# Performance work log

Measured on AMD Instinct MI355X. Metric: run time of the kernel, lower is better.

## Reference

```python
import jax, jax.numpy as jnp
import numpy as np

B, H, W, C = 4, 128, 128, 256
D_MODEL, NH = 512, 8
DH = D_MODEL // NH  # 64


def setup_inputs() -> dict:
    key = jax.random.key(0)
    ks = jax.random.split(key, 5)
    s = lambda fan_in: 1.0 / np.sqrt(fan_in)
    return {
        "x": jax.random.normal(ks[0], (B, H, W, C), jnp.float32),
        "Wq": jax.random.normal(ks[1], (C, D_MODEL), jnp.float32) * s(C),
        "bq": jnp.zeros((D_MODEL,), jnp.float32),
        "Wk": jax.random.normal(ks[2], (C, D_MODEL), jnp.float32) * s(C),
        "bk": jnp.zeros((D_MODEL,), jnp.float32),
        "Wv": jax.random.normal(ks[3], (C, D_MODEL), jnp.float32) * s(C),
        "bv": jnp.zeros((D_MODEL,), jnp.float32),
        "Wo": jax.random.normal(ks[4], (D_MODEL, C), jnp.float32) * s(D_MODEL),
        "bo": jnp.zeros((C,), jnp.float32),
    }


def reference(x, Wq, bq, Wk, bk, Wv, bv, Wo, bo):
    # Axial multi-head attention along axis 1 (H), W axis is batched.
    b, h, w, _ = x.shape
    q = (x @ Wq + bq).reshape(b, h, w, NH, DH) * (DH ** -0.5)
    k = (x @ Wk + bk).reshape(b, h, w, NH, DH)
    v = (x @ Wv + bv).reshape(b, h, w, NH, DH)
    # scores over the H axis: [B, Nh, W, H, H]
    scores = jnp.einsum("bxwnd,bywnd->bnwxy", q, k)
    probs = jax.nn.softmax(scores, axis=-1)
    # [B, H, W, Nh, DH] -> [B, H, W, d_model]
    out = jnp.einsum("bnwxy,bywnd->bxwnd", probs, v).reshape(b, h, w, D_MODEL)
    # Wo projection; original combines to [B,W,H,C] then permutes back to [B,H,W,C],
    # which is equivalent to applying Wo directly here. Dropout is identity at inference.
    return out @ Wo + bo
```

## Files before the change

kernel.cpp:

```cpp
#include <hip/hip_runtime.h>

typedef unsigned short u16;
typedef __attribute__((ext_vector_type(8))) short bf16x8;
typedef __attribute__((ext_vector_type(8))) unsigned short u16x8;
typedef __attribute__((ext_vector_type(4))) float f32x4;

#define DEVI static __device__ __forceinline__

DEVI u16 f2b(float f) {
  unsigned u = __builtin_bit_cast(unsigned, f);
  return (u16)((u + 0x7FFFu + ((u >> 16) & 1u)) >> 16);
}

DEVI void gload_lds16(const void* g, void* l) {
  __builtin_amdgcn_global_load_lds(
      (const __attribute__((address_space(1))) unsigned int*)g,
      (__attribute__((address_space(3))) unsigned int*)l, 16, 0, 0);
}


__global__ __launch_bounds__(256) void prep_x(const float* __restrict__ x, u16* __restrict__ xb) {
  const int n8 = 65536 * 256 / 8;
  int i = blockIdx.x * blockDim.x + threadIdx.x;
  for (; i < n8; i += gridDim.x * blockDim.x) {
    const float4* p = (const float4*)x + (size_t)i * 2;
    float4 a = p[0], b = p[1];
    u16x8 r;
    r[0] = f2b(a.x); r[1] = f2b(a.y); r[2] = f2b(a.z); r[3] = f2b(a.w);
    r[4] = f2b(b.x); r[5] = f2b(b.y); r[6] = f2b(b.z); r[7] = f2b(b.w);
    *(u16x8*)(xb + (size_t)i * 8) = r;
  }
}

__global__ __launch_bounds__(256) void prep_w(
    const float* __restrict__ Wq, const float* __restrict__ Wk,
    const float* __restrict__ Wv, const float* __restrict__ Wo,
    const float* __restrict__ bq, const float* __restrict__ bk, const float* __restrict__ bv,
    u16* __restrict__ wqkvT, u16* __restrict__ woT, float* __restrict__ bqkv) {
  const int NW1 = 1536 * 256, NW2 = 256 * 512;
  const int total = NW1 + NW2 + 1536;
  int i = blockIdx.x * blockDim.x + threadIdx.x;
  for (; i < total; i += gridDim.x * blockDim.x) {
    if (i < NW1) {
      int nn = i >> 8, kk = i & 255;
      float v;
      if (nn < 512)       v = Wq[kk * 512 + nn] * 0.125f;
      else if (nn < 1024) v = Wk[kk * 512 + (nn - 512)];
      else                v = Wv[kk * 512 + (nn - 1024)];
      wqkvT[i] = f2b(v);
    } else if (i < NW1 + NW2) {
      int j = i - NW1;
      int nn = j >> 9, kk = j & 511;
      woT[j] = f2b(Wo[kk * 256 + nn]);
    } else {
      int j = i - NW1 - NW2;
      bqkv[j] = (j < 512) ? bq[j] * 0.125f : (j < 1024 ? bk[j - 512] : bv[j - 1024]);
    }
  }
}


template <int KK, bool OUT_BF16>
__global__ __launch_bounds__(1024) void gemm256(
    const u16* __restrict__ A, const u16* __restrict__ Bt,
    const float* __restrict__ bias, void* __restrict__ Cv, int N) {
  constexpr int NT = KK / 64;
  __shared__ u16 smem[65536];
  const int tid = threadIdx.x;
  const int lane = tid & 63, wid = tid >> 6;
  const int nTn = N >> 8;
  const int qx = gridDim.x >> 3;
  const int wg = (blockIdx.x & 7) * qx + (blockIdx.x >> 3);
  const long m0 = (long)(wg / nTn) * 256;
  const long n0 = (long)(wg % nTn) * 256;
  const int wr = wid >> 2, wc = wid & 3;
  const int hi = lane >> 4, lo = lane & 15;
  const u16* Ab = A + m0 * KK;
  const u16* Bb = Bt + n0 * KK;
  const int srow_ = tid >> 3;
  const int schunk = tid & 7;

  f32x4 acc[4][4];
#pragma unroll
  for (int mi = 0; mi < 4; ++mi)
#pragma unroll
    for (int ni = 0; ni < 4; ++ni) acc[mi][ni] = f32x4{0.f, 0.f, 0.f, 0.f};

  auto stage = [&](int t) {
    u16* base = &smem[(t & 1) * 32768];
    const int kt = t * 64;
#pragma unroll
    for (int j = 0; j < 2; ++j) {
      int row = j * 128 + srow_;
      int colE = (schunk ^ (row & 7)) << 3;
      gload_lds16(Ab + (long)row * KK + kt + colE, &base[(j * 1024 + tid) * 8]);
    }
#pragma unroll
    for (int j = 0; j < 2; ++j) {
      int row = j * 128 + srow_;
      int colE = (schunk ^ (row & 7)) << 3;
      gload_lds16(Bb + (long)row * KK + kt + colE, &base[16384 + (j * 1024 + tid) * 8]);
    }
  };

  stage(0);
#pragma unroll
  for (int t = 0; t < NT; ++t) {
    if (t + 1 < NT) {
      stage(t + 1);
      asm volatile("s_waitcnt vmcnt(4)" ::: "memory");
    } else {
      asm volatile("s_waitcnt vmcnt(0)" ::: "memory");
    }
    __builtin_amdgcn_sched_barrier(0);
    __builtin_amdgcn_s_barrier();
    const u16* aB = &smem[(t & 1) * 32768];
    const u16* bB = aB + 16384;
#pragma unroll
    for (int ks = 0; ks < 2; ++ks) {
      const int slot = ((hi + ks * 4) ^ (lo & 7)) << 3;
      bf16x8 af[4], bfr[4];
#pragma unroll
      for (int mi = 0; mi < 4; ++mi)
        af[mi] = *(const bf16x8*)&aB[(wr * 64 + mi * 16 + lo) * 64 + slot];
#pragma unroll
      for (int ni = 0; ni < 4; ++ni)
        bfr[ni] = *(const bf16x8*)&bB[(wc * 64 + ni * 16 + lo) * 64 + slot];
#pragma unroll
      for (int mi = 0; mi < 4; ++mi)
#pragma unroll
        for (int ni = 0; ni < 4; ++ni)
          acc[mi][ni] = __builtin_amdgcn_mfma_f32_16x16x32_bf16(af[mi], bfr[ni], acc[mi][ni], 0, 0, 0);
    }
    __builtin_amdgcn_sched_barrier(0);
    __builtin_amdgcn_s_barrier();
  }

  float bb[4];
#pragma unroll
  for (int ni = 0; ni < 4; ++ni) bb[ni] = bias[n0 + wc * 64 + ni * 16 + lo];

  if (OUT_BF16) {
    u16* Cg = (u16*)Cv;
#pragma unroll
    for (int mi = 0; mi < 4; ++mi)
#pragma unroll
      for (int ni = 0; ni < 4; ++ni) {
#pragma unroll
        for (int j = 0; j < 4; ++j) {
          int row = wr * 64 + mi * 16 + hi * 4 + j;
          int chunk = (wc * 8 + ni * 2 + (lo >> 3)) ^ ((row >> 2) & 7);
          smem[row * 256 + chunk * 8 + (lo & 7)] = f2b(acc[mi][ni][j] + bb[ni]);
        }
      }
    __syncthreads();
#pragma unroll
    for (int it = 0; it < 8; ++it) {
      int idx = it * 1024 + tid;
      int row = idx >> 5, c = idx & 31;
      int cs = c ^ ((row >> 2) & 7);
      *(u16x8*)(Cg + (m0 + row) * N + n0 + c * 8) = *(const u16x8*)&smem[row * 256 + cs * 8];
    }
  } else {
    float* Cg = (float*)Cv;
#pragma unroll
    for (int mi = 0; mi < 4; ++mi)
#pragma unroll
      for (int ni = 0; ni < 4; ++ni) {
        long cg = n0 + wc * 64 + ni * 16 + lo;
#pragma unroll
        for (int j = 0; j < 4; ++j)
          Cg[(m0 + wr * 64 + mi * 16 + hi * 4 + j) * N + cg] = acc[mi][ni][j] + bb[ni];
      }
  }
}


__global__ __launch_bounds__(256) void attn_axial(const u16* __restrict__ qkv,
                                                  u16* __restrict__ ao) {
  __shared__ u16 smem[24576];
  u16* qld = smem;
  u16* kld = smem + 8192;
  u16* vt  = smem + 16384;
  u16* pld = smem;

  const int g = blockIdx.x;
  const int n = g & 7, w = (g >> 3) & 127, b = g >> 10;
  const int tid = threadIdx.x, lane = tid & 63, wid = tid >> 6;
  const size_t ystr = (size_t)128 * 1536;
  const size_t base = (size_t)(b * 16384 + w) * 1536;
  const size_t bq_ = base + n * 64;
  const size_t bk_ = base + 512 + n * 64;
  const size_t bv_ = base + 1024 + n * 64;
  const int srow = lane >> 3, sc = lane & 7;
  const int hi = lane >> 4, lo = lane & 15;

#pragma unroll
  for (int j = 0; j < 4; ++j) {
    int y = wid * 32 + j * 8 + srow;
    gload_lds16(qkv + bq_ + (size_t)y * ystr + sc * 8, &qld[(wid * 32 + j * 8) * 64]);
    gload_lds16(qkv + bk_ + (size_t)y * ystr + sc * 8, &kld[(wid * 32 + j * 8) * 64]);
  }
  {
    const int h2 = tid >> 6;
    const int yp = (tid & 63) * 2;
    const u16* g0 = qkv + bv_ + (size_t)yp * ystr + h2 * 16;
    u16x8 a0 = *(const u16x8*)g0;
    u16x8 a1 = *(const u16x8*)(g0 + 8);
    u16x8 c0 = *(const u16x8*)(g0 + ystr);
    u16x8 c1 = *(const u16x8*)(g0 + ystr + 8);
    unsigned* vt32 = (unsigned*)vt;
#pragma unroll
    for (int e = 0; e < 8; ++e) {
      vt32[(h2 * 16 + e) * 64 + (yp >> 1)]     = (unsigned)a0[e] | ((unsigned)c0[e] << 16);
      vt32[(h2 * 16 + 8 + e) * 64 + (yp >> 1)] = (unsigned)a1[e] | ((unsigned)c1[e] << 16);
    }
  }
  __syncthreads();

  f32x4 s[2][8];
#pragma unroll
  for (int mi = 0; mi < 2; ++mi)
#pragma unroll
    for (int ni = 0; ni < 8; ++ni) s[mi][ni] = f32x4{0.f, 0.f, 0.f, 0.f};
#pragma unroll
  for (int ks = 0; ks < 2; ++ks) {
    bf16x8 aq[2];
#pragma unroll
    for (int mi = 0; mi < 2; ++mi)
      aq[mi] = *(const bf16x8*)&qld[(wid * 32 + mi * 16 + lo) * 64 + hi * 8 + ks * 32];
#pragma unroll
    for (int ni = 0; ni < 8; ++ni) {
      bf16x8 bk2 = *(const bf16x8*)&kld[(ni * 16 + lo) * 64 + hi * 8 + ks * 32];
#pragma unroll
      for (int mi = 0; mi < 2; ++mi)
        s[mi][ni] = __builtin_amdgcn_mfma_f32_16x16x32_bf16(aq[mi], bk2, s[mi][ni], 0, 0, 0);
    }
  }
  __syncthreads();

  float rinv[2][4];
  u16* pw = &pld[wid * 32 * 128];
#pragma unroll
  for (int mi = 0; mi < 2; ++mi) {
#pragma unroll
    for (int j = 0; j < 4; ++j) {
      float m = s[mi][0][j];
#pragma unroll
      for (int ni = 1; ni < 8; ++ni) m = fmaxf(m, s[mi][ni][j]);
#pragma unroll
      for (int d = 1; d < 16; d <<= 1) m = fmaxf(m, __shfl_xor(m, d, 64));
      float sum = 0.f;
#pragma unroll
      for (int ni = 0; ni < 8; ++ni) {
        float e = exp2f((s[mi][ni][j] - m) * 1.44269504f);
        s[mi][ni][j] = e;
        sum += e;
      }
#pragma unroll
      for (int d = 1; d < 16; d <<= 1) sum += __shfl_xor(sum, d, 64);
      rinv[mi][j] = 1.f / sum;
      const int q = mi * 16 + hi * 4 + j;
#pragma unroll
      for (int ni = 0; ni < 8; ++ni)
        pw[q * 128 + ni * 16 + lo] = f2b(s[mi][ni][j]);
    }
  }

  f32x4 o[2][4];
#pragma unroll
  for (int mi = 0; mi < 2; ++mi)
#pragma unroll
    for (int ni = 0; ni < 4; ++ni) o[mi][ni] = f32x4{0.f, 0.f, 0.f, 0.f};
#pragma unroll
  for (int ks = 0; ks < 4; ++ks) {
    bf16x8 ap[2];
#pragma unroll
    for (int mi = 0; mi < 2; ++mi)
      ap[mi] = *(const bf16x8*)&pw[(mi * 16 + lo) * 128 + hi * 8 + ks * 32];
#pragma unroll
    for (int ni = 0; ni < 4; ++ni) {
      bf16x8 bv2 = *(const bf16x8*)&vt[(ni * 16 + lo) * 128 + hi * 8 + ks * 32];
#pragma unroll
      for (int mi = 0; mi < 2; ++mi)
        o[mi][ni] = __builtin_amdgcn_mfma_f32_16x16x32_bf16(ap[mi], bv2, o[mi][ni], 0, 0, 0);
    }
  }

#pragma unroll
  for (int mi = 0; mi < 2; ++mi)
#pragma unroll
    for (int j = 0; j < 4; ++j) {
      const int q = wid * 32 + mi * 16 + hi * 4 + j;
      const size_t obase = ((size_t)(b * 16384 + q * 128 + w)) * 512 + (size_t)n * 64;
#pragma unroll
      for (int ni = 0; ni < 4; ++ni)
        ao[obase + ni * 16 + lo] = f2b(o[mi][ni][j] * rinv[mi][j]);
    }
}


extern "C" void kernel_launch(void* const* d_in, const int* in_sizes, int n_in,
                              void* d_out, int out_size, void* d_ws, size_t ws_size,
                              hipStream_t stream) {
  (void)in_sizes; (void)n_in; (void)out_size; (void)ws_size;
  const float* x  = (const float*)d_in[0];
  const float* Wq = (const float*)d_in[1];
  const float* bq = (const float*)d_in[2];
  const float* Wk = (const float*)d_in[3];
  const float* bk = (const float*)d_in[4];
  const float* Wv = (const float*)d_in[5];
  const float* bv = (const float*)d_in[6];
  const float* Wo = (const float*)d_in[7];
  const float* bo = (const float*)d_in[8];
  float* out = (float*)d_out;

  char* ws = (char*)d_ws;
  const size_t MiB = (size_t)1 << 20;
  u16* qkv   = (u16*)ws;
  u16* xb    = (u16*)(ws + 192 * MiB);
  u16* wqkvT = (u16*)(ws + 224 * MiB);
  u16* woT   = wqkvT + 1536 * 256;
  float* bqkv = (float*)(woT + 256 * 512);

  prep_x<<<2048, 256, 0, stream>>>(x, xb);
  prep_w<<<512, 256, 0, stream>>>(Wq, Wk, Wv, Wo, bq, bk, bv, wqkvT, woT, bqkv);

  gemm256<256, true><<<1536, 1024, 0, stream>>>(xb, wqkvT, bqkv, qkv, 1536);
  attn_axial<<<4096, 256, 0, stream>>>(qkv, (u16*)out);
  gemm256<512, false><<<256, 1024, 0, stream>>>((const u16*)out, woT, bo, out, 256);
}
```

Baseline: 224.1 us.

## Swizzle attention LDS layouts, load Q straight to registers, add MFMA priority

The axial attention kernel now loads Q fragments directly from global memory into registers instead of staging them in LDS. K, V-transpose and P tiles are stored in LDS with an XOR swizzle on 16-byte chunks to reduce bank conflicts on the MFMA fragment reads and the softmax writes. s_setprio is raised around the MFMA loops. This trades the async global_load_lds path for register-staged loads with more address arithmetic and higher register pressure, and the uncoalesced per-lane Q reads may cost global bandwidth.

```diff
diff --git a/kernel.cpp b/kernel.cpp
--- a/kernel.cpp
+++ b/kernel.cpp
@@ -179,10 +179,9 @@
 __global__ __launch_bounds__(256) void attn_axial(const u16* __restrict__ qkv,
                                                   u16* __restrict__ ao) {
   __shared__ u16 smem[24576];
-  u16* qld = smem;
-  u16* kld = smem + 8192;
+  u16* kld = smem;
+  u16* pld = smem;
   u16* vt  = smem + 16384;
-  u16* pld = smem;
 
   const int g = blockIdx.x;
   const int n = g & 7, w = (g >> 3) & 127, b = g >> 10;
@@ -192,28 +191,48 @@
   const size_t bq_ = base + n * 64;
   const size_t bk_ = base + 512 + n * 64;
   const size_t bv_ = base + 1024 + n * 64;
-  const int srow = lane >> 3, sc = lane & 7;
   const int hi = lane >> 4, lo = lane & 15;
 
-#pragma unroll
-  for (int j = 0; j < 4; ++j) {
-    int y = wid * 32 + j * 8 + srow;
-    gload_lds16(qkv + bq_ + (size_t)y * ystr + sc * 8, &qld[(wid * 32 + j * 8) * 64]);
-    gload_lds16(qkv + bk_ + (size_t)y * ystr + sc * 8, &kld[(wid * 32 + j * 8) * 64]);
-  }
+  u16x8 kreg[4];
+  const int kr0 = tid >> 3, kc = tid & 7;
+#pragma unroll
+  for (int i = 0; i < 4; ++i)
+    kreg[i] = *(const u16x8*)(qkv + bk_ + (size_t)(i * 32 + kr0) * ystr + kc * 8);
+
+  u16x8 va0, va1, vc0, vc1;
+  const int vh2 = tid >> 6, vyp = (tid & 63) * 2;
   {
-    const int h2 = tid >> 6;
-    const int yp = (tid & 63) * 2;
-    const u16* g0 = qkv + bv_ + (size_t)yp * ystr + h2 * 16;
-    u16x8 a0 = *(const u16x8*)g0;
-    u16x8 a1 = *(const u16x8*)(g0 + 8);
-    u16x8 c0 = *(const u16x8*)(g0 + ystr);
-    u16x8 c1 = *(const u16x8*)(g0 + ystr + 8);
+    const u16* g0 = qkv + bv_ + (size_t)vyp * ystr + vh2 * 16;
+    va0 = *(const u16x8*)g0;
+    va1 = *(const u16x8*)(g0 + 8);
+    vc0 = *(const u16x8*)(g0 + ystr);
+    vc1 = *(const u16x8*)(g0 + ystr + 8);
+  }
+
+  bf16x8 aq[2][2];
+#pragma unroll
+  for (int mi = 0; mi < 2; ++mi)
+#pragma unroll
+    for (int ks = 0; ks < 2; ++ks)
+      aq[mi][ks] = *(const bf16x8*)(qkv + bq_ +
+          (size_t)(wid * 32 + mi * 16 + lo) * ystr + hi * 8 + ks * 32);
+
+#pragma unroll
+  for (int i = 0; i < 4; ++i) {
+    const int r = i * 32 + kr0;
+    *(u16x8*)&kld[r * 64 + ((kc ^ (r & 7)) << 3)] = kreg[i];
+  }
+  {
     unsigned* vt32 = (unsigned*)vt;
+    const int cch = vyp >> 3;
+    const int cw = (vyp >> 1) & 3;
 #pragma unroll
     for (int e = 0; e < 8; ++e) {
-      vt32[(h2 * 16 + e) * 64 + (yp >> 1)]     = (unsigned)a0[e] | ((unsigned)c0[e] << 16);
-      vt32[(h2 * 16 + 8 + e) * 64 + (yp >> 1)] = (unsigned)a1[e] | ((unsigned)c1[e] << 16);
+      const int d0 = vh2 * 16 + e, d1 = vh2 * 16 + 8 + e;
+      const int c0s = (cch & 8) | ((cch & 7) ^ (d0 & 7));
+      const int c1s = (cch & 8) | ((cch & 7) ^ (d1 & 7));
+      vt32[d0 * 64 + c0s * 4 + cw] = (unsigned)va0[e] | ((unsigned)vc0[e] << 16);
+      vt32[d1 * 64 + c1s * 4 + cw] = (unsigned)va1[e] | ((unsigned)vc1[e] << 16);
     }
   }
   __syncthreads();
@@ -223,24 +242,22 @@
   for (int mi = 0; mi < 2; ++mi)
 #pragma unroll
     for (int ni = 0; ni < 8; ++ni) s[mi][ni] = f32x4{0.f, 0.f, 0.f, 0.f};
+  __builtin_amdgcn_s_setprio(1);
 #pragma unroll
   for (int ks = 0; ks < 2; ++ks) {
-    bf16x8 aq[2];
-#pragma unroll
-    for (int mi = 0; mi < 2; ++mi)
-      aq[mi] = *(const bf16x8*)&qld[(wid * 32 + mi * 16 + lo) * 64 + hi * 8 + ks * 32];
 #pragma unroll
     for (int ni = 0; ni < 8; ++ni) {
-      bf16x8 bk2 = *(const bf16x8*)&kld[(ni * 16 + lo) * 64 + hi * 8 + ks * 32];
+      const int kr = ni * 16 + lo;
+      bf16x8 kf = *(const bf16x8*)&kld[kr * 64 + (((hi + ks * 4) ^ (kr & 7)) << 3)];
 #pragma unroll
       for (int mi = 0; mi < 2; ++mi)
-        s[mi][ni] = __builtin_amdgcn_mfma_f32_16x16x32_bf16(aq[mi], bk2, s[mi][ni], 0, 0, 0);
-    }
-  }
+        s[mi][ni] = __builtin_amdgcn_mfma_f32_16x16x32_bf16(aq[mi][ks], kf, s[mi][ni], 0, 0, 0);
+    }
+  }
+  __builtin_amdgcn_s_setprio(0);
   __syncthreads();
 
   float rinv[2][4];
-  u16* pw = &pld[wid * 32 * 128];
 #pragma unroll
   for (int mi = 0; mi < 2; ++mi) {
 #pragma unroll
@@ -260,10 +277,14 @@
 #pragma unroll
       for (int d = 1; d < 16; d <<= 1) sum += __shfl_xor(sum, d, 64);
       rinv[mi][j] = 1.f / sum;
-      const int q = mi * 16 + hi * 4 + j;
-#pragma unroll
-      for (int ni = 0; ni < 8; ++ni)
-        pw[q * 128 + ni * 16 + lo] = f2b(s[mi][ni][j]);
+      const int q = wid * 32 + mi * 16 + hi * 4 + j;
+#pragma unroll
+      for (int ni = 0; ni < 8; ++ni) {
+        const int yp = ni * 16 + lo;
+        const int cch = yp >> 3;
+        const int cs = (cch & 8) | ((cch & 7) ^ (q & 7));
+        pld[q * 128 + cs * 8 + (yp & 7)] = f2b(s[mi][ni][j]);
+      }
     }
   }
 
@@ -272,20 +293,28 @@
   for (int mi = 0; mi < 2; ++mi)
 #pragma unroll
     for (int ni = 0; ni < 4; ++ni) o[mi][ni] = f32x4{0.f, 0.f, 0.f, 0.f};
+  __builtin_amdgcn_s_setprio(1);
 #pragma unroll
   for (int ks = 0; ks < 4; ++ks) {
+    const int cch = hi + ks * 4;
     bf16x8 ap[2];
 #pragma unroll
-    for (int mi = 0; mi < 2; ++mi)
-      ap[mi] = *(const bf16x8*)&pw[(mi * 16 + lo) * 128 + hi * 8 + ks * 32];
+    for (int mi = 0; mi < 2; ++mi) {
+      const int pr = wid * 32 + mi * 16 + lo;
+      const int cs = (cch & 8) | ((cch & 7) ^ (pr & 7));
+      ap[mi] = *(const bf16x8*)&pld[pr * 128 + cs * 8];
+    }
 #pragma unroll
     for (int ni = 0; ni < 4; ++ni) {
-      bf16x8 bv2 = *(const bf16x8*)&vt[(ni * 16 + lo) * 128 + hi * 8 + ks * 32];
+      const int vr = ni * 16 + lo;
+      const int cs = (cch & 8) | ((cch & 7) ^ (vr & 7));
+      bf16x8 vf = *(const bf16x8*)&vt[vr * 128 + cs * 8];
 #pragma unroll
       for (int mi = 0; mi < 2; ++mi)
-        o[mi][ni] = __builtin_amdgcn_mfma_f32_16x16x32_bf16(ap[mi], bv2, o[mi][ni], 0, 0, 0);
-    }
-  }
+        o[mi][ni] = __builtin_amdgcn_mfma_f32_16x16x32_bf16(ap[mi], vf, o[mi][ni], 0, 0, 0);
+    }
+  }
+  __builtin_amdgcn_s_setprio(0);
 
 #pragma unroll
   for (int mi = 0; mi < 2; ++mi)
```

New measurement: 225.9 us. No clear change (+0.8%).
